# Performance work log

Hardware: AMD Instinct MI355X
Metric: run time of the kernel (lower is better)

Reference implementation:

```python
import jax, jax.numpy as jnp
import numpy as np

B = 16384          # batch
N = 24             # num_features / fields
CARD = 10000       # vocab per feature (all equal)
D = 16             # factor_dim
NI = N * (N - 1) // 2  # 276 pairwise interactions
H1, H2 = 128, 64


def setup_inputs() -> dict:
    key = jax.random.key(0)
    ks = jax.random.split(key, 10)
    x = jax.random.randint(ks[0], (B, N), 0, CARD, dtype=jnp.int32)
    # field-aware embedding table: E[f, id, field, :] is feature f's embedding w.r.t. field
    E = jax.random.normal(ks[1], (N, CARD, N, D), dtype=jnp.float32) * 0.01
    Wlin = jax.random.normal(ks[2], (N, CARD), dtype=jnp.float32) * 0.01
    blin = jnp.zeros((1,), dtype=jnp.float32)
    W1 = jax.random.normal(ks[3], (NI, H1), dtype=jnp.float32) * (1.0 / np.sqrt(NI))
    b1 = jnp.zeros((H1,), dtype=jnp.float32)
    W2 = jax.random.normal(ks[4], (H1, H2), dtype=jnp.float32) * (1.0 / np.sqrt(H1))
    b2 = jnp.zeros((H2,), dtype=jnp.float32)
    W3 = jax.random.normal(ks[5], (H2, 1), dtype=jnp.float32) * (1.0 / np.sqrt(H2))
    b3 = jnp.zeros((1,), dtype=jnp.float32)
    return {"x": x, "E": E, "Wlin": Wlin, "blin": blin,
            "W1": W1, "b1": b1, "W2": W2, "b2": b2, "W3": W3, "b3": b3}


def reference(x, E, Wlin, blin, W1, b1, W2, b2, W3, b3):
    feat_idx = jnp.arange(N)[None, :]              # [1, N]
    # factors[b, i, j, :] = embedding of feature i (value x[b,i]) w.r.t. field j
    factors = E[feat_idx, x]                        # [B, N, N, D]
    # interactions[b, i, j] = <factors[b,i,j], factors[b,j,i]>
    inter = jnp.sum(factors * jnp.swapaxes(factors, 1, 2), axis=-1)  # [B, N, N]
    iu, ju = jnp.triu_indices(N, k=1)
    pairs = inter[:, iu, ju]                        # [B, NI] strict upper triangle, row-major
    # FCN (dropout inactive at inference): relu -> relu -> linear
    h = jax.nn.relu(pairs @ W1 + b1)
    h = jax.nn.relu(h @ W2 + b2)
    nn_out = h @ W3 + b3                            # [B, 1]
    lin_out = jnp.sum(Wlin[feat_idx, x], axis=1, keepdims=True) + blin  # [B, 1]
    return lin_out + nn_out
```

## Files before the change

kernel.cpp:

```cpp
#include <hip/hip_runtime.h>

#define BB   16384
#define NF   24
#define CARDN 10000
#define DD   16
#define NI   276
#define H1N  128
#define H2N  64

__global__ __launch_bounds__(256) void pairs_kernel(
    const int* __restrict__ x, const float* __restrict__ E,
    float* __restrict__ pairs)
{
    int tid = blockIdx.x * 256 + threadIdx.x;
    int b = tid / NI;
    int p = tid - b * NI;

    int i = 0, rem = p, cnt = NF - 1;
    while (rem >= cnt) { rem -= cnt; --cnt; ++i; }
    int j = i + 1 + rem;

    int xi = x[b * NF + i];
    int xj = x[b * NF + j];

    const float4* a = (const float4*)(E + ((size_t)i * CARDN + xi) * (NF * DD) + j * DD);
    const float4* c = (const float4*)(E + ((size_t)j * CARDN + xj) * (NF * DD) + i * DD);
    float4 a0 = a[0], a1 = a[1], a2 = a[2], a3 = a[3];
    float4 c0 = c[0], c1 = c[1], c2 = c[2], c3 = c[3];

    float s =
        a0.x*c0.x + a0.y*c0.y + a0.z*c0.z + a0.w*c0.w +
        a1.x*c1.x + a1.y*c1.y + a1.z*c1.z + a1.w*c1.w +
        a2.x*c2.x + a2.y*c2.y + a2.z*c2.z + a2.w*c2.w +
        a3.x*c3.x + a3.y*c3.y + a3.z*c3.z + a3.w*c3.w;

    pairs[tid] = s;
}

__global__ __launch_bounds__(256) void mlp_kernel(
    const float* __restrict__ pairs, const int* __restrict__ x,
    const float* __restrict__ Wlin, const float* __restrict__ blin,
    const float* __restrict__ W1, const float* __restrict__ b1,
    const float* __restrict__ W2, const float* __restrict__ b2,
    const float* __restrict__ W3, const float* __restrict__ b3,
    float* __restrict__ out)
{
    const int BT = 32;
    __shared__ float pairs_s[BT * NI];
    __shared__ float h1_s[BT * H1N];
    __shared__ float lin_s[BT];

    int tid = threadIdx.x;
    int b0 = blockIdx.x * BT;

    {
        const float4* src = (const float4*)(pairs + (size_t)b0 * NI);
        float4* dst = (float4*)pairs_s;
        for (int idx = tid; idx < BT * NI / 4; idx += 256) dst[idx] = src[idx];
    }
    if (tid < BT) {
        float l = blin[0] + b3[0];
        const int* xr = x + (size_t)(b0 + tid) * NF;
        #pragma unroll
        for (int i = 0; i < NF; ++i) l += Wlin[i * CARDN + xr[i]];
        lin_s[tid] = l;
    }
    __syncthreads();

    {
        int c4 = tid & 31;
        int sg = tid >> 5;
        float acc[4][4] = {};
        for (int p = 0; p < NI; ++p) {
            float4 w = *(const float4*)(W1 + p * H1N + c4 * 4);
            #pragma unroll
            for (int si = 0; si < 4; ++si) {
                float pr = pairs_s[(sg * 4 + si) * NI + p];
                acc[si][0] = fmaf(pr, w.x, acc[si][0]);
                acc[si][1] = fmaf(pr, w.y, acc[si][1]);
                acc[si][2] = fmaf(pr, w.z, acc[si][2]);
                acc[si][3] = fmaf(pr, w.w, acc[si][3]);
            }
        }
        float4 bb = *(const float4*)(b1 + c4 * 4);
        #pragma unroll
        for (int si = 0; si < 4; ++si) {
            float4 h;
            h.x = fmaxf(acc[si][0] + bb.x, 0.f);
            h.y = fmaxf(acc[si][1] + bb.y, 0.f);
            h.z = fmaxf(acc[si][2] + bb.z, 0.f);
            h.w = fmaxf(acc[si][3] + bb.w, 0.f);
            *(float4*)(h1_s + (sg * 4 + si) * H1N + c4 * 4) = h;
        }
    }
    __syncthreads();

    float* h2_s = pairs_s;
    {
        int c16 = tid & 15;
        int sg2 = tid >> 4;
        float acc[2][4] = {};
        for (int p = 0; p < H1N; ++p) {
            float4 w = *(const float4*)(W2 + p * H2N + c16 * 4);
            #pragma unroll
            for (int si = 0; si < 2; ++si) {
                float pr = h1_s[(sg2 * 2 + si) * H1N + p];
                acc[si][0] = fmaf(pr, w.x, acc[si][0]);
                acc[si][1] = fmaf(pr, w.y, acc[si][1]);
                acc[si][2] = fmaf(pr, w.z, acc[si][2]);
                acc[si][3] = fmaf(pr, w.w, acc[si][3]);
            }
        }
        float4 bb = *(const float4*)(b2 + c16 * 4);
        #pragma unroll
        for (int si = 0; si < 2; ++si) {
            int s = sg2 * 2 + si;
            float v0 = fmaxf(acc[si][0] + bb.x, 0.f);
            float v1 = fmaxf(acc[si][1] + bb.y, 0.f);
            float v2 = fmaxf(acc[si][2] + bb.z, 0.f);
            float v3 = fmaxf(acc[si][3] + bb.w, 0.f);
            int base = s * 65 + c16 * 4;
            h2_s[base + 0] = v0;
            h2_s[base + 1] = v1;
            h2_s[base + 2] = v2;
            h2_s[base + 3] = v3;
        }
    }
    __syncthreads();

    {
        int s  = tid >> 3;
        int ko = tid & 7;
        float r = 0.f;
        #pragma unroll
        for (int kk = 0; kk < 8; ++kk) {
            int k = ko * 8 + kk;
            r = fmaf(h2_s[s * 65 + k], W3[k], r);
        }
        r += __shfl_xor(r, 1);
        r += __shfl_xor(r, 2);
        r += __shfl_xor(r, 4);
        if (ko == 0) out[b0 + s] = r + lin_s[s];
    }
}

extern "C" void kernel_launch(void* const* d_in, const int* in_sizes, int n_in,
                              void* d_out, int out_size, void* d_ws, size_t ws_size,
                              hipStream_t stream) {
    const int*   x    = (const int*)  d_in[0];
    const float* E    = (const float*)d_in[1];
    const float* Wlin = (const float*)d_in[2];
    const float* blin = (const float*)d_in[3];
    const float* W1   = (const float*)d_in[4];
    const float* b1   = (const float*)d_in[5];
    const float* W2   = (const float*)d_in[6];
    const float* b2   = (const float*)d_in[7];
    const float* W3   = (const float*)d_in[8];
    const float* b3   = (const float*)d_in[9];
    float* out   = (float*)d_out;
    float* pairs = (float*)d_ws;

    pairs_kernel<<<(BB * NI) / 256, 256, 0, stream>>>(x, E, pairs);
    mlp_kernel<<<BB / 32, 256, 0, stream>>>(pairs, x, Wlin, blin,
                                            W1, b1, W2, b2, W3, b3, out);
}
```

Measured before the change: 132.4 us.

## Fuse pairwise interaction gather with MLP into a single kernel

Merges the pairs kernel and the MLP kernel into one kernel that handles 16 samples per block. For each sample it copies the full embedding rows of all 24 fields into shared memory with contiguous float4 loads, then computes the 276 dot products from shared memory. It then runs the three MLP layers on transposed, padded shared-memory buffers. This removes the global pairs intermediate and one launch, but the per-sample load/sync loop and the large shared-memory footprint reduce occupancy and may leave gather latency exposed.

```diff
diff --git a/kernel.cpp b/kernel.cpp
--- a/kernel.cpp
+++ b/kernel.cpp
@@ -1,145 +1,161 @@
 #include <hip/hip_runtime.h>
 
-#define BB   16384
-#define NF   24
+#define BB    16384
+#define NF    24
 #define CARDN 10000
-#define DD   16
-#define NI   276
-#define H1N  128
-#define H2N  64
+#define DD    16
+#define NI    276
+#define H1N   128
+#define H2N   64
+#define SB    16
+#define RSTR  392
+#define PSTR  17
+#define HSTR  17
 
-__global__ __launch_bounds__(256) void pairs_kernel(
+__global__ __launch_bounds__(256) void fanfm_fused_kernel(
     const int* __restrict__ x, const float* __restrict__ E,
-    float* __restrict__ pairs)
-{
-    int tid = blockIdx.x * 256 + threadIdx.x;
-    int b = tid / NI;
-    int p = tid - b * NI;
-
-    int i = 0, rem = p, cnt = NF - 1;
-    while (rem >= cnt) { rem -= cnt; --cnt; ++i; }
-    int j = i + 1 + rem;
-
-    int xi = x[b * NF + i];
-    int xj = x[b * NF + j];
-
-    const float4* a = (const float4*)(E + ((size_t)i * CARDN + xi) * (NF * DD) + j * DD);
-    const float4* c = (const float4*)(E + ((size_t)j * CARDN + xj) * (NF * DD) + i * DD);
-    float4 a0 = a[0], a1 = a[1], a2 = a[2], a3 = a[3];
-    float4 c0 = c[0], c1 = c[1], c2 = c[2], c3 = c[3];
-
-    float s =
-        a0.x*c0.x + a0.y*c0.y + a0.z*c0.z + a0.w*c0.w +
-        a1.x*c1.x + a1.y*c1.y + a1.z*c1.z + a1.w*c1.w +
-        a2.x*c2.x + a2.y*c2.y + a2.z*c2.z + a2.w*c2.w +
-        a3.x*c3.x + a3.y*c3.y + a3.z*c3.z + a3.w*c3.w;
-
-    pairs[tid] = s;
-}
-
-__global__ __launch_bounds__(256) void mlp_kernel(
-    const float* __restrict__ pairs, const int* __restrict__ x,
     const float* __restrict__ Wlin, const float* __restrict__ blin,
     const float* __restrict__ W1, const float* __restrict__ b1,
     const float* __restrict__ W2, const float* __restrict__ b2,
     const float* __restrict__ W3, const float* __restrict__ b3,
     float* __restrict__ out)
 {
-    const int BT = 32;
-    __shared__ float pairs_s[BT * NI];
-    __shared__ float h1_s[BT * H1N];
-    __shared__ float lin_s[BT];
+    __shared__ float rows_s[NF * RSTR];
+    __shared__ float pairsT[NI * PSTR];
+    __shared__ int   xs[SB * NF];
+    __shared__ float lin_s[SB];
 
-    int tid = threadIdx.x;
-    int b0 = blockIdx.x * BT;
+    float* h1T = rows_s;
+    float* h2T = rows_s + H1N * HSTR;
 
-    {
-        const float4* src = (const float4*)(pairs + (size_t)b0 * NI);
-        float4* dst = (float4*)pairs_s;
-        for (int idx = tid; idx < BT * NI / 4; idx += 256) dst[idx] = src[idx];
-    }
-    if (tid < BT) {
+    const int tid = threadIdx.x;
+    const int b0  = blockIdx.x * SB;
+
+    for (int idx = tid; idx < SB * NF; idx += 256) xs[idx] = x[b0 * NF + idx];
+    __syncthreads();
+
+    if (tid < SB) {
         float l = blin[0] + b3[0];
-        const int* xr = x + (size_t)(b0 + tid) * NF;
         #pragma unroll
-        for (int i = 0; i < NF; ++i) l += Wlin[i * CARDN + xr[i]];
+        for (int i = 0; i < NF; ++i) l += Wlin[i * CARDN + xs[tid * NF + i]];
         lin_s[tid] = l;
     }
-    __syncthreads();
 
+    int pi0, pj0, pi1 = -1, pj1 = -1;
     {
-        int c4 = tid & 31;
-        int sg = tid >> 5;
-        float acc[4][4] = {};
-        for (int p = 0; p < NI; ++p) {
-            float4 w = *(const float4*)(W1 + p * H1N + c4 * 4);
-            #pragma unroll
-            for (int si = 0; si < 4; ++si) {
-                float pr = pairs_s[(sg * 4 + si) * NI + p];
-                acc[si][0] = fmaf(pr, w.x, acc[si][0]);
-                acc[si][1] = fmaf(pr, w.y, acc[si][1]);
-                acc[si][2] = fmaf(pr, w.z, acc[si][2]);
-                acc[si][3] = fmaf(pr, w.w, acc[si][3]);
-            }
+        int i = 0, rem = tid, cnt = NF - 1;
+        while (rem >= cnt) { rem -= cnt; --cnt; ++i; }
+        pi0 = i; pj0 = i + 1 + rem;
+    }
+    if (tid + 256 < NI) {
+        int i = 0, rem = tid + 256, cnt = NF - 1;
+        while (rem >= cnt) { rem -= cnt; --cnt; ++i; }
+        pi1 = i; pj1 = i + 1 + rem;
+    }
+
+    for (int s = 0; s < SB; ++s) {
+        __syncthreads();
+        #pragma unroll
+        for (int k = 0; k < 9; ++k) {
+            int idx = tid + k * 256;
+            int r   = idx / 96;
+            int cq  = idx - r * 96;
+            const float4 v = *(const float4*)(E +
+                ((size_t)r * CARDN + xs[s * NF + r]) * (NF * DD) + cq * 4);
+            *(float4*)(rows_s + r * RSTR + cq * 4) = v;
         }
-        float4 bb = *(const float4*)(b1 + c4 * 4);
-        #pragma unroll
-        for (int si = 0; si < 4; ++si) {
-            float4 h;
-            h.x = fmaxf(acc[si][0] + bb.x, 0.f);
-            h.y = fmaxf(acc[si][1] + bb.y, 0.f);
-            h.z = fmaxf(acc[si][2] + bb.z, 0.f);
-            h.w = fmaxf(acc[si][3] + bb.w, 0.f);
-            *(float4*)(h1_s + (sg * 4 + si) * H1N + c4 * 4) = h;
+        __syncthreads();
+        {
+            const float4* a = (const float4*)(rows_s + pi0 * RSTR + pj0 * DD);
+            const float4* c = (const float4*)(rows_s + pj0 * RSTR + pi0 * DD);
+            float4 a0 = a[0], a1 = a[1], a2 = a[2], a3 = a[3];
+            float4 c0 = c[0], c1 = c[1], c2 = c[2], c3 = c[3];
+            float d =
+                a0.x*c0.x + a0.y*c0.y + a0.z*c0.z + a0.w*c0.w +
+                a1.x*c1.x + a1.y*c1.y + a1.z*c1.z + a1.w*c1.w +
+                a2.x*c2.x + a2.y*c2.y + a2.z*c2.z + a2.w*c2.w +
+                a3.x*c3.x + a3.y*c3.y + a3.z*c3.z + a3.w*c3.w;
+            pairsT[tid * PSTR + s] = d;
         }
-    }
-    __syncthreads();
-
-    float* h2_s = pairs_s;
-    {
-        int c16 = tid & 15;
-        int sg2 = tid >> 4;
-        float acc[2][4] = {};
-        for (int p = 0; p < H1N; ++p) {
-            float4 w = *(const float4*)(W2 + p * H2N + c16 * 4);
-            #pragma unroll
-            for (int si = 0; si < 2; ++si) {
-                float pr = h1_s[(sg2 * 2 + si) * H1N + p];
-                acc[si][0] = fmaf(pr, w.x, acc[si][0]);
-                acc[si][1] = fmaf(pr, w.y, acc[si][1]);
-                acc[si][2] = fmaf(pr, w.z, acc[si][2]);
-                acc[si][3] = fmaf(pr, w.w, acc[si][3]);
-            }
-        }
-        float4 bb = *(const float4*)(b2 + c16 * 4);
-        #pragma unroll
-        for (int si = 0; si < 2; ++si) {
-            int s = sg2 * 2 + si;
-            float v0 = fmaxf(acc[si][0] + bb.x, 0.f);
-            float v1 = fmaxf(acc[si][1] + bb.y, 0.f);
-            float v2 = fmaxf(acc[si][2] + bb.z, 0.f);
-            float v3 = fmaxf(acc[si][3] + bb.w, 0.f);
-            int base = s * 65 + c16 * 4;
-            h2_s[base + 0] = v0;
-            h2_s[base + 1] = v1;
-            h2_s[base + 2] = v2;
-            h2_s[base + 3] = v3;
+        if (pi1 >= 0) {
+            const float4* a = (const float4*)(rows_s + pi1 * RSTR + pj1 * DD);
+            const float4* c = (const float4*)(rows_s + pj1 * RSTR + pi1 * DD);
+            float4 a0 = a[0], a1 = a[1], a2 = a[2], a3 = a[3];
+            float4 c0 = c[0], c1 = c[1], c2 = c[2], c3 = c[3];
+            float d =
+                a0.x*c0.x + a0.y*c0.y + a0.z*c0.z + a0.w*c0.w +
+                a1.x*c1.x + a1.y*c1.y + a1.z*c1.z + a1.w*c1.w +
+                a2.x*c2.x + a2.y*c2.y + a2.z*c2.z + a2.w*c2.w +
+                a3.x*c3.x + a3.y*c3.y + a3.z*c3.z + a3.w*c3.w;
+            pairsT[(tid + 256) * PSTR + s] = d;
         }
     }
     __syncthreads();
 
     {
-        int s  = tid >> 3;
-        int ko = tid & 7;
+        const int c4 = tid & 31;
+        const int sg = tid >> 5;
+        float acc[2][4] = {};
+        #pragma unroll 4
+        for (int p = 0; p < NI; ++p) {
+            float4 w = *(const float4*)(W1 + p * H1N + c4 * 4);
+            float pr0 = pairsT[p * PSTR + sg * 2 + 0];
+            float pr1 = pairsT[p * PSTR + sg * 2 + 1];
+            acc[0][0] = fmaf(pr0, w.x, acc[0][0]);
+            acc[0][1] = fmaf(pr0, w.y, acc[0][1]);
+            acc[0][2] = fmaf(pr0, w.z, acc[0][2]);
+            acc[0][3] = fmaf(pr0, w.w, acc[0][3]);
+            acc[1][0] = fmaf(pr1, w.x, acc[1][0]);
+            acc[1][1] = fmaf(pr1, w.y, acc[1][1]);
+            acc[1][2] = fmaf(pr1, w.z, acc[1][2]);
+            acc[1][3] = fmaf(pr1, w.w, acc[1][3]);
+        }
+        float4 bb = *(const float4*)(b1 + c4 * 4);
+        #pragma unroll
+        for (int si = 0; si < 2; ++si) {
+            int s = sg * 2 + si;
+            h1T[(c4 * 4 + 0) * HSTR + s] = fmaxf(acc[si][0] + bb.x, 0.f);
+            h1T[(c4 * 4 + 1) * HSTR + s] = fmaxf(acc[si][1] + bb.y, 0.f);
+            h1T[(c4 * 4 + 2) * HSTR + s] = fmaxf(acc[si][2] + bb.z, 0.f);
+            h1T[(c4 * 4 + 3) * HSTR + s] = fmaxf(acc[si][3] + bb.w, 0.f);
+        }
+    }
+    __syncthreads();
+
+    {
+        const int c16 = tid & 15;
+        const int sg2 = tid >> 4;
+        float acc[4] = {};
+        #pragma unroll 4
+        for (int p = 0; p < H1N; ++p) {
+            float4 w = *(const float4*)(W2 + p * H2N + c16 * 4);
+            float pr = h1T[p * HSTR + sg2];
+            acc[0] = fmaf(pr, w.x, acc[0]);
+            acc[1] = fmaf(pr, w.y, acc[1]);
+            acc[2] = fmaf(pr, w.z, acc[2]);
+            acc[3] = fmaf(pr, w.w, acc[3]);
+        }
+        float4 bb = *(const float4*)(b2 + c16 * 4);
+        h2T[(c16 * 4 + 0) * HSTR + sg2] = fmaxf(acc[0] + bb.x, 0.f);
+        h2T[(c16 * 4 + 1) * HSTR + sg2] = fmaxf(acc[1] + bb.y, 0.f);
+        h2T[(c16 * 4 + 2) * HSTR + sg2] = fmaxf(acc[2] + bb.z, 0.f);
+        h2T[(c16 * 4 + 3) * HSTR + sg2] = fmaxf(acc[3] + bb.w, 0.f);
+    }
+    __syncthreads();
+
+    {
+        const int s  = tid >> 4;
+        const int ko = tid & 15;
         float r = 0.f;
         #pragma unroll
-        for (int kk = 0; kk < 8; ++kk) {
-            int k = ko * 8 + kk;
-            r = fmaf(h2_s[s * 65 + k], W3[k], r);
+        for (int kk = 0; kk < 4; ++kk) {
+            int k = ko * 4 + kk;
+            r = fmaf(h2T[k * HSTR + s], W3[k], r);
         }
         r += __shfl_xor(r, 1);
         r += __shfl_xor(r, 2);
         r += __shfl_xor(r, 4);
+        r += __shfl_xor(r, 8);
         if (ko == 0) out[b0 + s] = r + lin_s[s];
     }
 }
@@ -157,10 +173,8 @@
     const float* b2   = (const float*)d_in[7];
     const float* W3   = (const float*)d_in[8];
     const float* b3   = (const float*)d_in[9];
-    float* out   = (float*)d_out;
-    float* pairs = (float*)d_ws;
+    float* out = (float*)d_out;
 
-    pairs_kernel<<<(BB * NI) / 256, 256, 0, stream>>>(x, E, pairs);
-    mlp_kernel<<<BB / 32, 256, 0, stream>>>(pairs, x, Wlin, blin,
-                                            W1, b1, W2, b2, W3, b3, out);
+    fanfm_fused_kernel<<<BB / SB, 256, 0, stream>>>(
+        x, E, Wlin, blin, W1, b1, W2, b2, W3, b3, out);
 }
```

Measured after the change: 146.9 us. 1.11x slower.
